# Performance work log

Hardware: AMD Instinct MI355X
Metric: run time of the kernel (lower is better)

## Reference

```python
import jax, jax.numpy as jnp
import numpy as np

GRID = 480  # grid extent for both x and y voxel indices


def setup_inputs() -> dict:
    key = jax.random.key(0)
    k = jax.random.split(key, 8)
    B, N, FD, H1, H2, D = 4, 100000, 3, 128, 256, 64
    scale = 0.05
    pt_fea = jax.random.normal(k[0], (B, N, FD), dtype=jnp.float32)
    xy_ind = jax.random.randint(k[1], (B, N, 2), 0, GRID, dtype=jnp.int32)
    W1 = jax.random.normal(k[2], (FD, H1), dtype=jnp.float32) * scale
    b1 = jnp.zeros((H1,), dtype=jnp.float32)
    W2 = jax.random.normal(k[3], (H1, H2), dtype=jnp.float32) * scale
    b2 = jnp.zeros((H2,), dtype=jnp.float32)
    W3 = jax.random.normal(k[4], (H2, D), dtype=jnp.float32) * scale
    b3 = jnp.zeros((D,), dtype=jnp.float32)
    return {"pt_fea": pt_fea, "xy_ind": xy_ind, "W1": W1, "b1": b1,
            "W2": W2, "b2": b2, "W3": W3, "b3": b3}


def reference(pt_fea, xy_ind, W1, b1, W2, b2, W3, b3):
    B, N, FD = pt_fea.shape
    flat = pt_fea.reshape(B * N, FD)
    # pad xy_ind with batch id -> (b, x, y) per point
    bidx = jnp.repeat(jnp.arange(B, dtype=xy_ind.dtype), N)
    xy = xy_ind.reshape(B * N, 2)
    # lexicographic linear encoding so sorted linear order == torch.unique(dim=0) row order
    lin = (bidx.astype(jnp.int32) * GRID + xy[:, 0]) * GRID + xy[:, 1]
    unq_lin, unq_inv = jnp.unique(lin, return_inverse=True)
    M = int(unq_lin.shape[0])  # concrete: indices are concrete (eager unique)
    unq = jnp.stack([unq_lin // (GRID * GRID),
                     (unq_lin // GRID) % GRID,
                     unq_lin % GRID], axis=1)
    # per-point MLP: 3 -> 128 -> 256 -> 64
    h = jax.nn.relu(flat @ W1 + b1)
    h = jax.nn.relu(h @ W2 + b2)
    feat = h @ W3 + b3
    # scatter_max pooling per unique voxel
    pooled = jax.ops.segment_max(feat, unq_inv.reshape(-1), num_segments=M)
    return unq, pooled
```

## Files before the change

### kernel.cpp

```cpp
#include <hip/hip_runtime.h>
#include <hip/hip_bf16.h>

#define GRIDW 480
#define CELLS_PER_B (GRIDW*GRIDW)
#define NCELL (4*CELLS_PER_B)
#define NPTS  400000
#define NPB   100000
#define H1D 128
#define H2D 256
#define DD 64
#define SCAN_BLK 900
#define NTILE 6250
#define GRIDP 512
#define NSUB  25000
#define CNT_NB 1563

typedef unsigned short u16;
typedef __attribute__((ext_vector_type(8))) short bf16x8;
typedef __attribute__((ext_vector_type(4))) float f32x4;
typedef __attribute__((ext_vector_type(4))) unsigned u32x4;
typedef __attribute__((ext_vector_type(2))) unsigned u32x2;

static __device__ __forceinline__ u16 f2bf(float f){
  unsigned u = __float_as_uint(f);
  unsigned r = u + 0x7FFFu + ((u>>16)&1u);
  return (u16)(r>>16);
}
static __device__ __forceinline__ float bf2f(u16 b){
  return __uint_as_float(((unsigned)b) << 16);
}
static __device__ __forceinline__ unsigned cvt_pk_bf16(float lo, float hi){
  unsigned r;
  asm("v_cvt_pk_bf16_f32 %0, %1, %2" : "=v"(r) : "v"(lo), "v"(hi));
  return r;
}

static __device__ __forceinline__ void pack_one(int e, const float* W2, const float* W3,
                                                u16* bp2, u16* bp3){
  if (e < 32768){
    int j = e & 7, c = (e>>3)&15, ko = (e>>7)&15, n = e>>11;
    bp2[e] = f2bf(W2[(ko*8+j)*H2D + n*16 + c]);
  } else {
    int e3 = e - 32768;
    int j = e3 & 7, c = (e3>>3)&15, ko = (e3>>7)&31, n = e3>>12;
    bp3[e3] = f2bf(W3[(ko*8+j)*DD + n*16 + c]);
  }
}

__global__ void k_countpack(const int* __restrict__ xy, unsigned* __restrict__ counts,
                            const float* __restrict__ W2, const float* __restrict__ W3,
                            u16* __restrict__ bp2, u16* __restrict__ bp3){
  int b = blockIdx.x;
  if (b < CNT_NB){
    int p = b*256 + threadIdx.x;
    if (p < NPTS){
      int bb = p / NPB;
      int x = xy[2*p], y = xy[2*p+1];
      atomicAdd(&counts[(bb*GRIDW + x)*GRIDW + y], 1u);
    }
  } else {
    int e = (b - CNT_NB)*256 + threadIdx.x;
    if (e < 49152) pack_one(e, W2, W3, bp2, bp3);
  }
}

__global__ void k_scan2(const unsigned* __restrict__ counts,
                        unsigned* __restrict__ rankF, unsigned* __restrict__ rankC,
                        unsigned* __restrict__ bsumF, unsigned* __restrict__ bsumC){
  __shared__ unsigned shF[256], shC[256];
  int tid = threadIdx.x;
  int base = blockIdx.x*1024 + tid*4;
  unsigned c0=counts[base], c1=counts[base+1], c2=counts[base+2], c3=counts[base+3];
  unsigned f0=c0?1u:0u, f1=c1?1u:0u, f2=c2?1u:0u, f3=c3?1u:0u;
  unsigned sF=f0+f1+f2+f3, sC=c0+c1+c2+c3;
  shF[tid]=sF; shC[tid]=sC; __syncthreads();
  for (int off=1; off<256; off<<=1){
    unsigned tF = (tid>=off) ? shF[tid-off] : 0u;
    unsigned tC = (tid>=off) ? shC[tid-off] : 0u;
    __syncthreads();
    shF[tid] += tF; shC[tid] += tC;
    __syncthreads();
  }
  unsigned eF = shF[tid]-sF, eC = shC[tid]-sC;
  if (tid==255){ bsumF[blockIdx.x]=shF[255]; bsumC[blockIdx.x]=shC[255]; }
  rankF[base]=eF; rankF[base+1]=eF+f0; rankF[base+2]=eF+f0+f1; rankF[base+3]=eF+f0+f1+f2;
  rankC[base]=eC; rankC[base+1]=eC+c0; rankC[base+2]=eC+c0+c1; rankC[base+3]=eC+c0+c1+c2;
}

__global__ void k_scan_bsum2(unsigned* __restrict__ bsumF, unsigned* __restrict__ bsumC){
  __shared__ unsigned shF[1024], shC[1024];
  int tid = threadIdx.x;
  unsigned vF = (tid<SCAN_BLK) ? bsumF[tid] : 0u;
  unsigned vC = (tid<SCAN_BLK) ? bsumC[tid] : 0u;
  shF[tid]=vF; shC[tid]=vC; __syncthreads();
  for (int off=1; off<1024; off<<=1){
    unsigned tF = (tid>=off) ? shF[tid-off] : 0u;
    unsigned tC = (tid>=off) ? shC[tid-off] : 0u;
    __syncthreads();
    shF[tid] += tF; shC[tid] += tC;
    __syncthreads();
  }
  if (tid<SCAN_BLK){ bsumF[tid]=shF[tid]-vF; bsumC[tid]=shC[tid]-vC; }
}

__global__ void k_emit2(const unsigned* __restrict__ counts,
                        unsigned* __restrict__ rankF, unsigned* __restrict__ rankC,
                        const unsigned* __restrict__ bsumF, const unsigned* __restrict__ bsumC,
                        float* __restrict__ out){
  int i = blockIdx.x*256 + threadIdx.x;
  if (i >= NCELL) return;
  unsigned rF = rankF[i] + bsumF[i>>10];
  unsigned rC = rankC[i] + bsumC[i>>10];
  rankF[i] = rF; rankC[i] = rC;
  unsigned c = counts[i];
  if (c){
    int b = i / CELLS_PER_B;
    int rem = i - b*CELLS_PER_B;
    int x = rem / GRIDW;
    int y = rem - x*GRIDW;
    float* o = out + 3u*rF;
    o[0]=(float)b; o[1]=(float)x; o[2]=(float)y;
  }
}

__global__ void k_scatterp(const int* __restrict__ xy, unsigned* __restrict__ cursor,
                           const unsigned* __restrict__ rankF,
                           unsigned* __restrict__ perm, unsigned* __restrict__ vox){
  int p = blockIdx.x*256 + threadIdx.x;
  if (p >= NPTS) return;
  int b = p / NPB;
  int x = xy[2*p], y = xy[2*p+1];
  int cell = (b*GRIDW+x)*GRIDW + y;
  unsigned slot = atomicAdd(&cursor[cell], 1u);
  perm[slot] = (unsigned)p;
  vox[slot]  = rankF[cell];
}

__global__ __launch_bounds__(256,1) void k_mlpp(
    const float* __restrict__ pt, const unsigned* __restrict__ perm,
    const unsigned* __restrict__ vox,
    const u16* __restrict__ bp2, const u16* __restrict__ bp3,
    const float* __restrict__ W1, const float* __restrict__ b1,
    const float* __restrict__ b2, const float* __restrict__ b3,
    float* __restrict__ outp,
    unsigned* __restrict__ pvf, unsigned* __restrict__ pvl,
    u16* __restrict__ pmf, u16* __restrict__ pml)
{
  __shared__ __attribute__((aligned(16))) u16 h1s[64*128];
  __shared__ __attribute__((aligned(16))) u16 h2s[2][64*64];
  __shared__ __attribute__((aligned(16))) float in_s[192];
  __shared__ unsigned vox_s[64];

  const int tid  = threadIdx.x;
  const int lane = tid & 63;
  const int w    = tid >> 6;
  const int g    = lane >> 4;
  const int p    = lane & 15;
  const int wn   = w & 1;
  const int wp   = w >> 1;
  const int oct  = tid & 15;

  bf16x8 wf2[32];
  #pragma unroll
  for (int c=0;c<4;++c)
    #pragma unroll
    for (int nn=0;nn<2;++nn)
      #pragma unroll
      for (int t=0;t<4;++t){
        int ngl = c*4 + 2*wn + nn;
        wf2[(c*2+nn)*4+t] = *(const bf16x8*)(bp2 + (((ngl*16 + t*4 + g)*16) + p)*8);
      }
  bf16x8 wf3[16];
  #pragma unroll
  for (int c=0;c<4;++c)
    #pragma unroll
    for (int t2=0;t2<2;++t2)
      #pragma unroll
      for (int dn=0;dn<2;++dn){
        int s = c*2+t2, dt = 2*wn+dn;
        wf3[(c*2+t2)*2+dn] = *(const bf16x8*)(bp3 + (((dt*32 + s*4 + g)*16) + p)*8);
      }
  f32x4 W1p[3][2], b1p[2];
  #pragma unroll
  for (int f=0;f<3;++f){
    W1p[f][0] = *(const f32x4*)(W1 + f*H1D + oct*8);
    W1p[f][1] = *(const f32x4*)(W1 + f*H1D + oct*8 + 4);
  }
  b1p[0] = *(const f32x4*)(b1 + oct*8);
  b1p[1] = *(const f32x4*)(b1 + oct*8 + 4);
  f32x4 b2p[4][2];
  #pragma unroll
  for (int c=0;c<4;++c)
    #pragma unroll
    for (int nn=0;nn<2;++nn)
      b2p[c][nn] = *(const f32x4*)(b2 + c*64 + (2*wn+nn)*16 + g*4);
  f32x4 b3p[2];
  #pragma unroll
  for (int dn=0;dn<2;++dn)
    b3p[dn] = *(const f32x4*)(b3 + (2*wn+dn)*16 + g*4);

  int tile = blockIdx.x;
  unsigned pmN = 0;
  float pf0=0.f, pf1=0.f, pf2=0.f;
  if (tid < 64){
    unsigned pm0 = perm[(size_t)tile*64 + tid];
    const float* q = pt + 3*(size_t)pm0;
    pf0 = q[0]; pf1 = q[1]; pf2 = q[2];
    if (tile + GRIDP < NTILE) pmN = perm[(size_t)(tile+GRIDP)*64 + tid];
  }

  for (; tile < NTILE; tile += GRIDP){
    if (tid < 64){ in_s[tid*3]=pf0; in_s[tid*3+1]=pf1; in_s[tid*3+2]=pf2; }
    unsigned vr = 0;
    if (tid < 64) vr = vox[(size_t)tile*64 + tid];
    __syncthreads();
    if (tid < 64 && tile + GRIDP < NTILE){
      const float* q = pt + 3*(size_t)pmN;
      pf0 = q[0]; pf1 = q[1]; pf2 = q[2];
    }
    unsigned pmN2 = 0;
    if (tid < 64 && tile + 2*GRIDP < NTILE)
      pmN2 = perm[(size_t)(tile+2*GRIDP)*64 + tid];

    #pragma unroll
    for (int q=0;q<4;++q){
      int row = q*16 + (tid>>4);
      float x0 = in_s[row*3+0], x1 = in_s[row*3+1], x2 = in_s[row*3+2];
      f32x4 a0 = b1p[0], a1 = b1p[1];
      #pragma unroll
      for (int i=0;i<4;++i){
        a0[i] = fmaf(x0, W1p[0][0][i], a0[i]);
        a1[i] = fmaf(x0, W1p[0][1][i], a1[i]);
        a0[i] = fmaf(x1, W1p[1][0][i], a0[i]);
        a1[i] = fmaf(x1, W1p[1][1][i], a1[i]);
        a0[i] = fmaf(x2, W1p[2][0][i], a0[i]);
        a1[i] = fmaf(x2, W1p[2][1][i], a1[i]);
        a0[i] = fmaxf(a0[i], 0.f);
        a1[i] = fmaxf(a1[i], 0.f);
      }
      u32x4 ov;
      ov[0] = cvt_pk_bf16(a0[0], a0[1]);
      ov[1] = cvt_pk_bf16(a0[2], a0[3]);
      ov[2] = cvt_pk_bf16(a1[0], a1[1]);
      ov[3] = cvt_pk_bf16(a1[2], a1[3]);
      unsigned byte = ((unsigned)row<<8) + (unsigned)oct*16u;
      byte ^= (unsigned)(row&7) << 4;
      *(u32x4*)((char*)h1s + byte) = ov;
    }
    if (tid < 64) vox_s[tid] = vr;
    __syncthreads();

    bf16x8 hf[2][4];
    #pragma unroll
    for (int pp=0;pp<2;++pp){
      int row = (2*wp+pp)*16 + p;
      #pragma unroll
      for (int t=0;t<4;++t){
        unsigned byte = ((unsigned)row<<8) + (unsigned)t*64u + (unsigned)g*16u;
        byte ^= (unsigned)(row&7) << 4;
        hf[pp][t] = *(const bf16x8*)((const char*)h1s + byte);
      }
    }

    f32x4 acc3[2][2];
    #pragma unroll
    for (int a=0;a<2;++a)
      #pragma unroll
      for (int b=0;b<2;++b){ acc3[a][b][0]=0.f; acc3[a][b][1]=0.f; acc3[a][b][2]=0.f; acc3[a][b][3]=0.f; }

    #pragma unroll
    for (int c=0;c<4;++c){
      f32x4 acc2[2][2];
      #pragma unroll
      for (int a=0;a<2;++a)
        #pragma unroll
        for (int b=0;b<2;++b){ acc2[a][b][0]=0.f; acc2[a][b][1]=0.f; acc2[a][b][2]=0.f; acc2[a][b][3]=0.f; }
      #pragma unroll
      for (int t=0;t<4;++t)
        #pragma unroll
        for (int nn=0;nn<2;++nn)
          #pragma unroll
          for (int pp=0;pp<2;++pp)
            acc2[nn][pp] = __builtin_amdgcn_mfma_f32_16x16x32_bf16(
                wf2[(c*2+nn)*4+t], hf[pp][t], acc2[nn][pp], 0, 0, 0);
      u16* h2 = h2s[c & 1];
      #pragma unroll
      for (int nn=0;nn<2;++nn)
        #pragma unroll
        for (int pp=0;pp<2;++pp){
          int point = (2*wp+pp)*16 + p;
          float e0 = fmaxf(acc2[nn][pp][0] + b2p[c][nn][0], 0.f);
          float e1 = fmaxf(acc2[nn][pp][1] + b2p[c][nn][1], 0.f);
          float e2 = fmaxf(acc2[nn][pp][2] + b2p[c][nn][2], 0.f);
          float e3 = fmaxf(acc2[nn][pp][3] + b2p[c][nn][3], 0.f);
          u32x2 o2; o2[0] = cvt_pk_bf16(e0, e1); o2[1] = cvt_pk_bf16(e2, e3);
          unsigned byte = (unsigned)point*128u + (unsigned)((2*wn+nn)*32 + g*8);
          byte ^= (unsigned)(point&7) << 4;
          *(u32x2*)((char*)h2 + byte) = o2;
        }
      __syncthreads();
      #pragma unroll
      for (int t2=0;t2<2;++t2){
        bf16x8 h2f[2];
        #pragma unroll
        for (int pp=0;pp<2;++pp){
          int point = (2*wp+pp)*16 + p;
          unsigned byte = (unsigned)point*128u + (unsigned)t2*64u + (unsigned)g*16u;
          byte ^= (unsigned)(point&7) << 4;
          h2f[pp] = *(const bf16x8*)((const char*)h2 + byte);
        }
        #pragma unroll
        for (int dn=0;dn<2;++dn)
          #pragma unroll
          for (int pp=0;pp<2;++pp)
            acc3[dn][pp] = __builtin_amdgcn_mfma_f32_16x16x32_bf16(
                wf3[(c*2+t2)*2+dn], h2f[pp], acc3[dn][pp], 0, 0, 0);
      }
    }

    #pragma unroll
    for (int dn=0;dn<2;++dn)
      #pragma unroll
      for (int pp=0;pp<2;++pp){
        int point = (2*wp+pp)*16 + p;
        float e0 = acc3[dn][pp][0] + b3p[dn][0];
        float e1 = acc3[dn][pp][1] + b3p[dn][1];
        float e2 = acc3[dn][pp][2] + b3p[dn][2];
        float e3 = acc3[dn][pp][3] + b3p[dn][3];
        u32x2 o2; o2[0] = cvt_pk_bf16(e0, e1); o2[1] = cvt_pk_bf16(e2, e3);
        unsigned byte = (unsigned)point*128u + (unsigned)((2*wn+dn)*32 + g*8);
        byte ^= (unsigned)(point&7) << 4;
        *(u32x2*)((char*)h2s[0] + byte) = o2;
      }
    __syncthreads();

    {
      int st = tile*4 + w;
      float val[16]; unsigned vid[16];
      #pragma unroll
      for (int r=0;r<16;++r){
        int row = w*16 + r;
        unsigned byte = (unsigned)row*128u + (unsigned)lane*2u;
        byte ^= (unsigned)(row&7) << 4;
        val[r] = bf2f(*(const u16*)((const char*)h2s[0] + byte));
        vid[r] = vox_s[row];
      }
      float m = val[0];
      unsigned vprev = vid[0];
      int runstart = 0;
      #pragma unroll
      for (int r=1;r<16;++r){
        if (vid[r] != vprev){
          if (runstart == 0){
            pmf[(size_t)st*64 + lane] = (u16)(__float_as_uint(m)>>16);
            if (lane==0) pvf[st] = vprev;
          } else {
            outp[(size_t)vprev*64 + lane] = m;
          }
          m = val[r]; runstart = r; vprev = vid[r];
        } else m = fmaxf(m, val[r]);
      }
      pml[(size_t)st*64 + lane] = (u16)(__float_as_uint(m)>>16);
      if (lane==0) pvl[st] = vprev;
      if (runstart == 0){
        pmf[(size_t)st*64 + lane] = (u16)(__float_as_uint(m)>>16);
        if (lane==0) pvf[st] = vprev;
      }
    }
    __syncthreads();
    pmN = pmN2;
  }
}

__global__ __launch_bounds__(256) void k_fixup(
    const unsigned* __restrict__ pvf, const unsigned* __restrict__ pvl,
    const u16* __restrict__ pmf, const u16* __restrict__ pml,
    float* __restrict__ outp){
  int t  = blockIdx.x*4 + (threadIdx.x>>6);
  int ch = threadIdx.x & 63;
  if (t >= NSUB) return;
  unsigned vf = pvf[t], vl = pvl[t];
  if (t == 0 || pvl[t-1] != vf){
    float m = bf2f(pmf[(size_t)t*64 + ch]);
    if (vl == vf){
      m = fmaxf(m, bf2f(pml[(size_t)t*64 + ch]));
      int k = t+1;
      while (k < NSUB && pvf[k] == vf){
        m = fmaxf(m, bf2f(pmf[(size_t)k*64 + ch]));
        if (pvl[k] != vf) break;
        m = fmaxf(m, bf2f(pml[(size_t)k*64 + ch]));
        ++k;
      }
    }
    outp[(size_t)vf*64 + ch] = m;
  }
  if (vl != vf){
    float m = bf2f(pml[(size_t)t*64 + ch]);
    int k = t+1;
    while (k < NSUB && pvf[k] == vl){
      m = fmaxf(m, bf2f(pmf[(size_t)k*64 + ch]));
      if (pvl[k] != vl) break;
      m = fmaxf(m, bf2f(pml[(size_t)k*64 + ch]));
      ++k;
    }
    outp[(size_t)vl*64 + ch] = m;
  }
}

extern "C" void kernel_launch(void* const* d_in, const int* in_sizes, int n_in,
                              void* d_out, int out_size, void* d_ws, size_t ws_size,
                              hipStream_t stream){
  const float* pt = (const float*)d_in[0];
  const int*   xy = (const int*)d_in[1];
  const float* W1 = (const float*)d_in[2];
  const float* b1 = (const float*)d_in[3];
  const float* W2 = (const float*)d_in[4];
  const float* b2 = (const float*)d_in[5];
  const float* W3 = (const float*)d_in[6];
  const float* b3 = (const float*)d_in[7];
  float* out = (float*)d_out;

  int M = out_size / 67;
  float* outp = out + 3*(size_t)M;

  unsigned* counts = (unsigned*)d_ws;
  unsigned* rankF  = counts + NCELL;
  unsigned* rankC  = rankF + NCELL;
  unsigned* bsumF  = rankC + NCELL;
  unsigned* bsumC  = bsumF + 1024;
  unsigned* perm   = bsumC + 1024;
  unsigned* vox    = perm + NPTS;
  unsigned* pvf    = vox + NPTS;
  unsigned* pvl    = pvf + NSUB;
  u16* bp2 = (u16*)(pvl + NSUB);
  u16* bp3 = bp2 + 32768;
  u16* pmf = bp3 + 16384;
  u16* pml = pmf + (size_t)NSUB*64;

  hipMemsetAsync(counts, 0, NCELL*sizeof(unsigned), stream);
  k_countpack  <<<CNT_NB+192, 256, 0, stream>>>(xy, counts, W2, W3, bp2, bp3);
  k_scan2      <<<SCAN_BLK, 256, 0, stream>>>(counts, rankF, rankC, bsumF, bsumC);
  k_scan_bsum2 <<<1, 1024, 0, stream>>>(bsumF, bsumC);
  k_emit2      <<<NCELL/256, 256, 0, stream>>>(counts, rankF, rankC, bsumF, bsumC, out);
  k_scatterp   <<<(NPTS+255)/256, 256, 0, stream>>>(xy, rankC, rankF, perm, vox);
  k_mlpp       <<<GRIDP, 256, 0, stream>>>(pt, perm, vox, bp2, bp3, W1, b1, b2, b3,
                                           outp, pvf, pvl, pmf, pml);
  k_fixup      <<<NSUB/4, 256, 0, stream>>>(pvf, pvl, pmf, pml, outp);
}
```

Measured before the change: 178.9 us.

## Move W3 fragments and bias constants to LDS to allow two blocks per CU

Layer-3 weight fragments and the W1/b1/b2/b3 constants were held in registers for the whole persistent loop. They are now staged once into shared memory and re-read from LDS inside the tile loop, and launch bounds go from 1 to 2 blocks per CU. The aim is to cut VGPR pressure so two blocks can be resident and hide latency. The cost is extra LDS traffic per tile (about 48KB of shared memory per block plus repeated fragment loads). The grid stays at 512 persistent blocks, so the higher occupancy may not be fully used.

```diff
diff --git a/kernel.cpp b/kernel.cpp
--- a/kernel.cpp
+++ b/kernel.cpp
@@ -136,7 +136,7 @@
   vox[slot]  = rankF[cell];
 }
 
-__global__ __launch_bounds__(256,1) void k_mlpp(
+__global__ __launch_bounds__(256,2) void k_mlpp(
     const float* __restrict__ pt, const unsigned* __restrict__ perm,
     const unsigned* __restrict__ vox,
     const u16* __restrict__ bp2, const u16* __restrict__ bp3,
@@ -148,6 +148,8 @@
 {
   __shared__ __attribute__((aligned(16))) u16 h1s[64*128];
   __shared__ __attribute__((aligned(16))) u16 h2s[2][64*64];
+  __shared__ __attribute__((aligned(16))) u16 w3s[16384];
+  __shared__ __attribute__((aligned(16))) float cf[832];
   __shared__ __attribute__((aligned(16))) float in_s[192];
   __shared__ unsigned vox_s[64];
 
@@ -160,6 +162,17 @@
   const int wp   = w >> 1;
   const int oct  = tid & 15;
 
+  for (int i = tid; i < 2048; i += 256)
+    *(u32x4*)((char*)w3s + i*16) = *(const u32x4*)((const char*)bp3 + i*16);
+  for (int i = tid; i < 832; i += 256){
+    float v;
+    if (i < 384) v = W1[i];
+    else if (i < 512) v = b1[i-384];
+    else if (i < 768) v = b2[i-512];
+    else v = b3[i-768];
+    cf[i] = v;
+  }
+
   bf16x8 wf2[32];
   #pragma unroll
   for (int c=0;c<4;++c)
@@ -170,34 +183,6 @@
         int ngl = c*4 + 2*wn + nn;
         wf2[(c*2+nn)*4+t] = *(const bf16x8*)(bp2 + (((ngl*16 + t*4 + g)*16) + p)*8);
       }
-  bf16x8 wf3[16];
-  #pragma unroll
-  for (int c=0;c<4;++c)
-    #pragma unroll
-    for (int t2=0;t2<2;++t2)
-      #pragma unroll
-      for (int dn=0;dn<2;++dn){
-        int s = c*2+t2, dt = 2*wn+dn;
-        wf3[(c*2+t2)*2+dn] = *(const bf16x8*)(bp3 + (((dt*32 + s*4 + g)*16) + p)*8);
-      }
-  f32x4 W1p[3][2], b1p[2];
-  #pragma unroll
-  for (int f=0;f<3;++f){
-    W1p[f][0] = *(const f32x4*)(W1 + f*H1D + oct*8);
-    W1p[f][1] = *(const f32x4*)(W1 + f*H1D + oct*8 + 4);
-  }
-  b1p[0] = *(const f32x4*)(b1 + oct*8);
-  b1p[1] = *(const f32x4*)(b1 + oct*8 + 4);
-  f32x4 b2p[4][2];
-  #pragma unroll
-  for (int c=0;c<4;++c)
-    #pragma unroll
-    for (int nn=0;nn<2;++nn)
-      b2p[c][nn] = *(const f32x4*)(b2 + c*64 + (2*wn+nn)*16 + g*4);
-  f32x4 b3p[2];
-  #pragma unroll
-  for (int dn=0;dn<2;++dn)
-    b3p[dn] = *(const f32x4*)(b3 + (2*wn+dn)*16 + g*4);
 
   int tile = blockIdx.x;
   unsigned pmN = 0;
@@ -208,6 +193,7 @@
     pf0 = q[0]; pf1 = q[1]; pf2 = q[2];
     if (tile + GRIDP < NTILE) pmN = perm[(size_t)(tile+GRIDP)*64 + tid];
   }
+  __syncthreads();
 
   for (; tile < NTILE; tile += GRIDP){
     if (tid < 64){ in_s[tid*3]=pf0; in_s[tid*3+1]=pf1; in_s[tid*3+2]=pf2; }
@@ -222,30 +208,40 @@
     if (tid < 64 && tile + 2*GRIDP < NTILE)
       pmN2 = perm[(size_t)(tile+2*GRIDP)*64 + tid];
 
-    #pragma unroll
-    for (int q=0;q<4;++q){
-      int row = q*16 + (tid>>4);
-      float x0 = in_s[row*3+0], x1 = in_s[row*3+1], x2 = in_s[row*3+2];
-      f32x4 a0 = b1p[0], a1 = b1p[1];
-      #pragma unroll
-      for (int i=0;i<4;++i){
-        a0[i] = fmaf(x0, W1p[0][0][i], a0[i]);
-        a1[i] = fmaf(x0, W1p[0][1][i], a1[i]);
-        a0[i] = fmaf(x1, W1p[1][0][i], a0[i]);
-        a1[i] = fmaf(x1, W1p[1][1][i], a1[i]);
-        a0[i] = fmaf(x2, W1p[2][0][i], a0[i]);
-        a1[i] = fmaf(x2, W1p[2][1][i], a1[i]);
-        a0[i] = fmaxf(a0[i], 0.f);
-        a1[i] = fmaxf(a1[i], 0.f);
-      }
-      u32x4 ov;
-      ov[0] = cvt_pk_bf16(a0[0], a0[1]);
-      ov[1] = cvt_pk_bf16(a0[2], a0[3]);
-      ov[2] = cvt_pk_bf16(a1[0], a1[1]);
-      ov[3] = cvt_pk_bf16(a1[2], a1[3]);
-      unsigned byte = ((unsigned)row<<8) + (unsigned)oct*16u;
-      byte ^= (unsigned)(row&7) << 4;
-      *(u32x4*)((char*)h1s + byte) = ov;
+    {
+      f32x4 w1v[3][2], b1v[2];
+      #pragma unroll
+      for (int f=0;f<3;++f){
+        w1v[f][0] = *(const f32x4*)&cf[f*128 + oct*8];
+        w1v[f][1] = *(const f32x4*)&cf[f*128 + oct*8 + 4];
+      }
+      b1v[0] = *(const f32x4*)&cf[384 + oct*8];
+      b1v[1] = *(const f32x4*)&cf[384 + oct*8 + 4];
+      #pragma unroll
+      for (int q=0;q<4;++q){
+        int row = q*16 + (tid>>4);
+        float x0 = in_s[row*3+0], x1 = in_s[row*3+1], x2 = in_s[row*3+2];
+        f32x4 a0 = b1v[0], a1 = b1v[1];
+        #pragma unroll
+        for (int i=0;i<4;++i){
+          a0[i] = fmaf(x0, w1v[0][0][i], a0[i]);
+          a1[i] = fmaf(x0, w1v[0][1][i], a1[i]);
+          a0[i] = fmaf(x1, w1v[1][0][i], a0[i]);
+          a1[i] = fmaf(x1, w1v[1][1][i], a1[i]);
+          a0[i] = fmaf(x2, w1v[2][0][i], a0[i]);
+          a1[i] = fmaf(x2, w1v[2][1][i], a1[i]);
+          a0[i] = fmaxf(a0[i], 0.f);
+          a1[i] = fmaxf(a1[i], 0.f);
+        }
+        u32x4 ov;
+        ov[0] = cvt_pk_bf16(a0[0], a0[1]);
+        ov[1] = cvt_pk_bf16(a0[2], a0[3]);
+        ov[2] = cvt_pk_bf16(a1[0], a1[1]);
+        ov[3] = cvt_pk_bf16(a1[2], a1[3]);
+        unsigned byte = ((unsigned)row<<8) + (unsigned)oct*16u;
+        byte ^= (unsigned)(row&7) << 4;
+        *(u32x4*)((char*)h1s + byte) = ov;
+      }
     }
     if (tid < 64) vox_s[tid] = vr;
     __syncthreads();
@@ -285,23 +281,31 @@
                 wf2[(c*2+nn)*4+t], hf[pp][t], acc2[nn][pp], 0, 0, 0);
       u16* h2 = h2s[c & 1];
       #pragma unroll
-      for (int nn=0;nn<2;++nn)
+      for (int nn=0;nn<2;++nn){
+        f32x4 b2v = *(const f32x4*)&cf[512 + c*64 + (2*wn+nn)*16 + g*4];
         #pragma unroll
         for (int pp=0;pp<2;++pp){
           int point = (2*wp+pp)*16 + p;
-          float e0 = fmaxf(acc2[nn][pp][0] + b2p[c][nn][0], 0.f);
-          float e1 = fmaxf(acc2[nn][pp][1] + b2p[c][nn][1], 0.f);
-          float e2 = fmaxf(acc2[nn][pp][2] + b2p[c][nn][2], 0.f);
-          float e3 = fmaxf(acc2[nn][pp][3] + b2p[c][nn][3], 0.f);
+          float e0 = fmaxf(acc2[nn][pp][0] + b2v[0], 0.f);
+          float e1 = fmaxf(acc2[nn][pp][1] + b2v[1], 0.f);
+          float e2 = fmaxf(acc2[nn][pp][2] + b2v[2], 0.f);
+          float e3 = fmaxf(acc2[nn][pp][3] + b2v[3], 0.f);
           u32x2 o2; o2[0] = cvt_pk_bf16(e0, e1); o2[1] = cvt_pk_bf16(e2, e3);
           unsigned byte = (unsigned)point*128u + (unsigned)((2*wn+nn)*32 + g*8);
           byte ^= (unsigned)(point&7) << 4;
           *(u32x2*)((char*)h2 + byte) = o2;
         }
+      }
       __syncthreads();
       #pragma unroll
       for (int t2=0;t2<2;++t2){
-        bf16x8 h2f[2];
+        bf16x8 w3f[2], h2f[2];
+        #pragma unroll
+        for (int dn=0;dn<2;++dn){
+          int dt = 2*wn + dn;
+          unsigned wb = (unsigned)(((dt*32 + (c*2+t2)*4 + g)*16 + p)*16);
+          w3f[dn] = *(const bf16x8*)((const char*)w3s + wb);
+        }
         #pragma unroll
         for (int pp=0;pp<2;++pp){
           int point = (2*wp+pp)*16 + p;
@@ -314,24 +318,26 @@
           #pragma unroll
           for (int pp=0;pp<2;++pp)
             acc3[dn][pp] = __builtin_amdgcn_mfma_f32_16x16x32_bf16(
-                wf3[(c*2+t2)*2+dn], h2f[pp], acc3[dn][pp], 0, 0, 0);
+                w3f[dn], h2f[pp], acc3[dn][pp], 0, 0, 0);
       }
     }
 
     #pragma unroll
-    for (int dn=0;dn<2;++dn)
+    for (int dn=0;dn<2;++dn){
+      f32x4 b3v = *(const f32x4*)&cf[768 + (2*wn+dn)*16 + g*4];
       #pragma unroll
       for (int pp=0;pp<2;++pp){
         int point = (2*wp+pp)*16 + p;
-        float e0 = acc3[dn][pp][0] + b3p[dn][0];
-        float e1 = acc3[dn][pp][1] + b3p[dn][1];
-        float e2 = acc3[dn][pp][2] + b3p[dn][2];
-        float e3 = acc3[dn][pp][3] + b3p[dn][3];
+        float e0 = acc3[dn][pp][0] + b3v[0];
+        float e1 = acc3[dn][pp][1] + b3v[1];
+        float e2 = acc3[dn][pp][2] + b3v[2];
+        float e3 = acc3[dn][pp][3] + b3v[3];
         u32x2 o2; o2[0] = cvt_pk_bf16(e0, e1); o2[1] = cvt_pk_bf16(e2, e3);
         unsigned byte = (unsigned)point*128u + (unsigned)((2*wn+dn)*32 + g*8);
         byte ^= (unsigned)(point&7) << 4;
         *(u32x2*)((char*)h2s[0] + byte) = o2;
       }
+    }
     __syncthreads();
 
     {
```

New measurement: 155.5 us. 13.1% less time.

## Fuse emit and scatter kernels, double MLP tile to 128 points, stage W3 in LDS

Applied to the files above, without the earlier changes.

Merges the cell-emit and point-scatter kernels into one launch. The scatter now adds the block prefix sums on the fly, so the full rank arrays are no longer rewritten. The fused MLP kernel handles 128 points per tile with half as many blocks, and loads W3 fragments from shared memory instead of registers. This frees registers for the larger accumulator set, and the next tile's vox values are also prefetched. The cost is more LDS per block, a longer serial run-max loop, and fewer blocks across the CUs.

```diff
diff --git a/kernel.cpp b/kernel.cpp
--- a/kernel.cpp
+++ b/kernel.cpp
@@ -10,10 +10,11 @@
 #define H2D 256
 #define DD 64
 #define SCAN_BLK 900
-#define NTILE 6250
-#define GRIDP 512
-#define NSUB  25000
+#define NTILE2 3125
+#define GRIDP 256
+#define NSUB  12500
 #define CNT_NB 1563
+#define EMIT_NB 3600
 
 typedef unsigned short u16;
 typedef __attribute__((ext_vector_type(8))) short bf16x8;
@@ -103,37 +104,36 @@
   if (tid<SCAN_BLK){ bsumF[tid]=shF[tid]-vF; bsumC[tid]=shC[tid]-vC; }
 }
 
-__global__ void k_emit2(const unsigned* __restrict__ counts,
-                        unsigned* __restrict__ rankF, unsigned* __restrict__ rankC,
-                        const unsigned* __restrict__ bsumF, const unsigned* __restrict__ bsumC,
-                        float* __restrict__ out){
-  int i = blockIdx.x*256 + threadIdx.x;
-  if (i >= NCELL) return;
-  unsigned rF = rankF[i] + bsumF[i>>10];
-  unsigned rC = rankC[i] + bsumC[i>>10];
-  rankF[i] = rF; rankC[i] = rC;
-  unsigned c = counts[i];
-  if (c){
-    int b = i / CELLS_PER_B;
-    int rem = i - b*CELLS_PER_B;
-    int x = rem / GRIDW;
-    int y = rem - x*GRIDW;
-    float* o = out + 3u*rF;
-    o[0]=(float)b; o[1]=(float)x; o[2]=(float)y;
-  }
-}
-
-__global__ void k_scatterp(const int* __restrict__ xy, unsigned* __restrict__ cursor,
-                           const unsigned* __restrict__ rankF,
-                           unsigned* __restrict__ perm, unsigned* __restrict__ vox){
-  int p = blockIdx.x*256 + threadIdx.x;
-  if (p >= NPTS) return;
-  int b = p / NPB;
-  int x = xy[2*p], y = xy[2*p+1];
-  int cell = (b*GRIDW+x)*GRIDW + y;
-  unsigned slot = atomicAdd(&cursor[cell], 1u);
-  perm[slot] = (unsigned)p;
-  vox[slot]  = rankF[cell];
+__global__ void k_emitscatter(
+    const unsigned* __restrict__ counts,
+    const unsigned* __restrict__ rankF, unsigned* __restrict__ rankC,
+    const unsigned* __restrict__ bsumF, const unsigned* __restrict__ bsumC,
+    const int* __restrict__ xy,
+    unsigned* __restrict__ perm, unsigned* __restrict__ vox,
+    float* __restrict__ out){
+  int b = blockIdx.x;
+  if (b < EMIT_NB){
+    int i = b*256 + threadIdx.x;
+    if (counts[i]){
+      unsigned rF = rankF[i] + bsumF[i>>10];
+      int bb = i / CELLS_PER_B;
+      int rem = i - bb*CELLS_PER_B;
+      int x = rem / GRIDW;
+      int y = rem - x*GRIDW;
+      float* o = out + 3u*rF;
+      o[0]=(float)bb; o[1]=(float)x; o[2]=(float)y;
+    }
+  } else {
+    int p = (b - EMIT_NB)*256 + threadIdx.x;
+    if (p < NPTS){
+      int bb = p / NPB;
+      int x = xy[2*p], y = xy[2*p+1];
+      int cell = (bb*GRIDW+x)*GRIDW + y;
+      unsigned slot = atomicAdd(&rankC[cell], 1u) + bsumC[cell>>10];
+      perm[slot] = (unsigned)p;
+      vox[slot]  = rankF[cell] + bsumF[cell>>10];
+    }
+  }
 }
 
 __global__ __launch_bounds__(256,1) void k_mlpp(
@@ -146,10 +146,11 @@
     unsigned* __restrict__ pvf, unsigned* __restrict__ pvl,
     u16* __restrict__ pmf, u16* __restrict__ pml)
 {
-  __shared__ __attribute__((aligned(16))) u16 h1s[64*128];
-  __shared__ __attribute__((aligned(16))) u16 h2s[2][64*64];
-  __shared__ __attribute__((aligned(16))) float in_s[192];
-  __shared__ unsigned vox_s[64];
+  __shared__ __attribute__((aligned(16))) u16 h1s[128*128];
+  __shared__ __attribute__((aligned(16))) u16 h2s[2][128*64];
+  __shared__ __attribute__((aligned(16))) u16 w3s[16384];
+  __shared__ __attribute__((aligned(16))) float in_s[384];
+  __shared__ unsigned vox_s[128];
 
   const int tid  = threadIdx.x;
   const int lane = tid & 63;
@@ -160,6 +161,9 @@
   const int wp   = w >> 1;
   const int oct  = tid & 15;
 
+  for (int i = tid; i < 2048; i += 256)
+    *(u32x4*)((char*)w3s + i*16) = *(const u32x4*)((const char*)bp3 + i*16);
+
   bf16x8 wf2[32];
   #pragma unroll
   for (int c=0;c<4;++c)
@@ -169,16 +173,6 @@
       for (int t=0;t<4;++t){
         int ngl = c*4 + 2*wn + nn;
         wf2[(c*2+nn)*4+t] = *(const bf16x8*)(bp2 + (((ngl*16 + t*4 + g)*16) + p)*8);
-      }
-  bf16x8 wf3[16];
-  #pragma unroll
-  for (int c=0;c<4;++c)
-    #pragma unroll
-    for (int t2=0;t2<2;++t2)
-      #pragma unroll
-      for (int dn=0;dn<2;++dn){
-        int s = c*2+t2, dt = 2*wn+dn;
-        wf3[(c*2+t2)*2+dn] = *(const bf16x8*)(bp3 + (((dt*32 + s*4 + g)*16) + p)*8);
       }
   f32x4 W1p[3][2], b1p[2];
   #pragma unroll
@@ -200,30 +194,33 @@
     b3p[dn] = *(const f32x4*)(b3 + (2*wn+dn)*16 + g*4);
 
   int tile = blockIdx.x;
-  unsigned pmN = 0;
+  unsigned pmN = 0, vr = 0;
   float pf0=0.f, pf1=0.f, pf2=0.f;
-  if (tid < 64){
-    unsigned pm0 = perm[(size_t)tile*64 + tid];
+  if (tid < 128){
+    unsigned pm0 = perm[(size_t)tile*128 + tid];
     const float* q = pt + 3*(size_t)pm0;
     pf0 = q[0]; pf1 = q[1]; pf2 = q[2];
-    if (tile + GRIDP < NTILE) pmN = perm[(size_t)(tile+GRIDP)*64 + tid];
-  }
-
-  for (; tile < NTILE; tile += GRIDP){
-    if (tid < 64){ in_s[tid*3]=pf0; in_s[tid*3+1]=pf1; in_s[tid*3+2]=pf2; }
-    unsigned vr = 0;
-    if (tid < 64) vr = vox[(size_t)tile*64 + tid];
-    __syncthreads();
-    if (tid < 64 && tile + GRIDP < NTILE){
+    vr = vox[(size_t)tile*128 + tid];
+    if (tile + GRIDP < NTILE2) pmN = perm[(size_t)(tile+GRIDP)*128 + tid];
+  }
+  __syncthreads();
+
+  for (; tile < NTILE2; tile += GRIDP){
+    if (tid < 128){
+      in_s[tid*3]=pf0; in_s[tid*3+1]=pf1; in_s[tid*3+2]=pf2;
+      vox_s[tid]=vr;
+    }
+    __syncthreads();
+    float nf0=0.f, nf1=0.f, nf2=0.f; unsigned nvr=0, pmN2=0;
+    if (tid < 128 && tile + GRIDP < NTILE2){
       const float* q = pt + 3*(size_t)pmN;
-      pf0 = q[0]; pf1 = q[1]; pf2 = q[2];
-    }
-    unsigned pmN2 = 0;
-    if (tid < 64 && tile + 2*GRIDP < NTILE)
-      pmN2 = perm[(size_t)(tile+2*GRIDP)*64 + tid];
-
-    #pragma unroll
-    for (int q=0;q<4;++q){
+      nf0 = q[0]; nf1 = q[1]; nf2 = q[2];
+      nvr = vox[(size_t)(tile+GRIDP)*128 + tid];
+      if (tile + 2*GRIDP < NTILE2) pmN2 = perm[(size_t)(tile+2*GRIDP)*128 + tid];
+    }
+
+    #pragma unroll
+    for (int q=0;q<8;++q){
       int row = q*16 + (tid>>4);
       float x0 = in_s[row*3+0], x1 = in_s[row*3+1], x2 = in_s[row*3+2];
       f32x4 a0 = b1p[0], a1 = b1p[1];
@@ -247,13 +244,12 @@
       byte ^= (unsigned)(row&7) << 4;
       *(u32x4*)((char*)h1s + byte) = ov;
     }
-    if (tid < 64) vox_s[tid] = vr;
-    __syncthreads();
-
-    bf16x8 hf[2][4];
-    #pragma unroll
-    for (int pp=0;pp<2;++pp){
-      int row = (2*wp+pp)*16 + p;
+    __syncthreads();
+
+    bf16x8 hf[4][4];
+    #pragma unroll
+    for (int pp=0;pp<4;++pp){
+      int row = (4*wp+pp)*16 + p;
       #pragma unroll
       for (int t=0;t<4;++t){
         unsigned byte = ((unsigned)row<<8) + (unsigned)t*64u + (unsigned)g*16u;
@@ -262,33 +258,33 @@
       }
     }
 
-    f32x4 acc3[2][2];
+    f32x4 acc3[2][4];
     #pragma unroll
     for (int a=0;a<2;++a)
       #pragma unroll
-      for (int b=0;b<2;++b){ acc3[a][b][0]=0.f; acc3[a][b][1]=0.f; acc3[a][b][2]=0.f; acc3[a][b][3]=0.f; }
+      for (int b=0;b<4;++b){ acc3[a][b][0]=0.f; acc3[a][b][1]=0.f; acc3[a][b][2]=0.f; acc3[a][b][3]=0.f; }
 
     #pragma unroll
     for (int c=0;c<4;++c){
-      f32x4 acc2[2][2];
+      f32x4 acc2[2][4];
       #pragma unroll
       for (int a=0;a<2;++a)
         #pragma unroll
-        for (int b=0;b<2;++b){ acc2[a][b][0]=0.f; acc2[a][b][1]=0.f; acc2[a][b][2]=0.f; acc2[a][b][3]=0.f; }
+        for (int b=0;b<4;++b){ acc2[a][b][0]=0.f; acc2[a][b][1]=0.f; acc2[a][b][2]=0.f; acc2[a][b][3]=0.f; }
       #pragma unroll
       for (int t=0;t<4;++t)
         #pragma unroll
         for (int nn=0;nn<2;++nn)
           #pragma unroll
-          for (int pp=0;pp<2;++pp)
+          for (int pp=0;pp<4;++pp)
             acc2[nn][pp] = __builtin_amdgcn_mfma_f32_16x16x32_bf16(
                 wf2[(c*2+nn)*4+t], hf[pp][t], acc2[nn][pp], 0, 0, 0);
       u16* h2 = h2s[c & 1];
       #pragma unroll
       for (int nn=0;nn<2;++nn)
         #pragma unroll
-        for (int pp=0;pp<2;++pp){
-          int point = (2*wp+pp)*16 + p;
+        for (int pp=0;pp<4;++pp){
+          int point = (4*wp+pp)*16 + p;
           float e0 = fmaxf(acc2[nn][pp][0] + b2p[c][nn][0], 0.f);
           float e1 = fmaxf(acc2[nn][pp][1] + b2p[c][nn][1], 0.f);
           float e2 = fmaxf(acc2[nn][pp][2] + b2p[c][nn][2], 0.f);
@@ -301,10 +297,16 @@
       __syncthreads();
       #pragma unroll
       for (int t2=0;t2<2;++t2){
-        bf16x8 h2f[2];
-        #pragma unroll
-        for (int pp=0;pp<2;++pp){
-          int point = (2*wp+pp)*16 + p;
+        bf16x8 w3f[2], h2f[4];
+        #pragma unroll
+        for (int dn=0;dn<2;++dn){
+          int dt = 2*wn + dn;
+          unsigned wb = (unsigned)(((dt*32 + (c*2+t2)*4 + g)*16 + p)*16);
+          w3f[dn] = *(const bf16x8*)((const char*)w3s + wb);
+        }
+        #pragma unroll
+        for (int pp=0;pp<4;++pp){
+          int point = (4*wp+pp)*16 + p;
           unsigned byte = (unsigned)point*128u + (unsigned)t2*64u + (unsigned)g*16u;
           byte ^= (unsigned)(point&7) << 4;
           h2f[pp] = *(const bf16x8*)((const char*)h2 + byte);
@@ -312,17 +314,17 @@
         #pragma unroll
         for (int dn=0;dn<2;++dn)
           #pragma unroll
-          for (int pp=0;pp<2;++pp)
+          for (int pp=0;pp<4;++pp)
             acc3[dn][pp] = __builtin_amdgcn_mfma_f32_16x16x32_bf16(
-                wf3[(c*2+t2)*2+dn], h2f[pp], acc3[dn][pp], 0, 0, 0);
+                w3f[dn], h2f[pp], acc3[dn][pp], 0, 0, 0);
       }
     }
 
     #pragma unroll
     for (int dn=0;dn<2;++dn)
       #pragma unroll
-      for (int pp=0;pp<2;++pp){
-        int point = (2*wp+pp)*16 + p;
+      for (int pp=0;pp<4;++pp){
+        int point = (4*wp+pp)*16 + p;
         float e0 = acc3[dn][pp][0] + b3p[dn][0];
         float e1 = acc3[dn][pp][1] + b3p[dn][1];
         float e2 = acc3[dn][pp][2] + b3p[dn][2];
@@ -336,10 +338,10 @@
 
     {
       int st = tile*4 + w;
-      float val[16]; unsigned vid[16];
-      #pragma unroll
-      for (int r=0;r<16;++r){
-        int row = w*16 + r;
+      float val[32]; unsigned vid[32];
+      #pragma unroll
+      for (int r=0;r<32;++r){
+        int row = w*32 + r;
         unsigned byte = (unsigned)row*128u + (unsigned)lane*2u;
         byte ^= (unsigned)(row&7) << 4;
         val[r] = bf2f(*(const u16*)((const char*)h2s[0] + byte));
@@ -349,7 +351,7 @@
       unsigned vprev = vid[0];
       int runstart = 0;
       #pragma unroll
-      for (int r=1;r<16;++r){
+      for (int r=1;r<32;++r){
         if (vid[r] != vprev){
           if (runstart == 0){
             pmf[(size_t)st*64 + lane] = (u16)(__float_as_uint(m)>>16);
@@ -368,7 +370,7 @@
       }
     }
     __syncthreads();
-    pmN = pmN2;
+    pf0=nf0; pf1=nf1; pf2=nf2; vr=nvr; pmN=pmN2;
   }
 }
 
@@ -441,8 +443,8 @@
   k_countpack  <<<CNT_NB+192, 256, 0, stream>>>(xy, counts, W2, W3, bp2, bp3);
   k_scan2      <<<SCAN_BLK, 256, 0, stream>>>(counts, rankF, rankC, bsumF, bsumC);
   k_scan_bsum2 <<<1, 1024, 0, stream>>>(bsumF, bsumC);
-  k_emit2      <<<NCELL/256, 256, 0, stream>>>(counts, rankF, rankC, bsumF, bsumC, out);
-  k_scatterp   <<<(NPTS+255)/256, 256, 0, stream>>>(xy, rankC, rankF, perm, vox);
+  k_emitscatter<<<EMIT_NB+CNT_NB, 256, 0, stream>>>(counts, rankF, rankC, bsumF, bsumC,
+                                                    xy, perm, vox, out);
   k_mlpp       <<<GRIDP, 256, 0, stream>>>(pt, perm, vox, bp2, bp3, W1, b1, b2, b3,
                                            outp, pvf, pvl, pmf, pml);
   k_fixup      <<<NSUB/4, 256, 0, stream>>>(pvf, pvl, pmf, pml, outp);
```

New measurement: 161.5 us. -9.7%, faster.
